# Performance work log

Hardware: AMD Instinct MI355X
Metric: run time of the kernel (lower is better)

## Reference

```python
import jax, jax.numpy as jnp
import numpy as np

N = 100000
E = 1600000
D = 64


def setup_inputs() -> dict:
    key = jax.random.key(0)
    k1, k2 = jax.random.split(key)
    x = jax.random.normal(k1, (N, D), dtype=jnp.float32)
    lambda_ = jnp.ones((), dtype=jnp.float32)  # nn.Parameter init 1.0
    edge_index = jax.random.randint(k2, (2, E), 0, N, dtype=jnp.int64)
    return {"input": x, "lambda_": lambda_, "edge_index": edge_index}


def reference(input, lambda_, edge_index):
    # actual lambda = 1 + relu(lambda_)
    lam = 1.0 + jax.nn.relu(lambda_)
    v1 = (2.0 * lam - 2.0) / lam  # self-loop weight
    v2 = 2.0 / lam                # neighbor edge weight
    row = edge_index[0]
    col = edge_index[1]
    # SpMM: out[r] = v1 * x[r] + v2 * sum_{(r,c) in E} x[c]
    nbr = jax.ops.segment_sum(input[col], row, num_segments=N)  # [N, D]
    agg = v1 * input + v2 * nbr
    # row-sum normalization: rowsum[r] = v1 + v2 * deg(r)
    deg = jax.ops.segment_sum(jnp.ones((E,), dtype=input.dtype), row, num_segments=N)
    rowsum = v1 + v2 * deg  # [N]
    return agg / rowsum[:, None]
```

## Files before the change

### kernel.cpp

```cpp
#include <hip/hip_runtime.h>

#define NN 100000
#define NE 1600000
#define DD 64

#define RSH 9
#define RPB 512
#define NBUCK 196
#define CAP 8704
#define CH2 8192
#define EPB 16
#define NABLK ((NE + CH2 - 1) / CH2)
#define CONV_TOT (NN * DD / 8)

__device__ __forceinline__ void get_v(const float* __restrict__ lam_p, float& v1, float& v2) {
    float l = lam_p[0];
    float lam = 1.0f + (l > 0.0f ? l : 0.0f);
    v1 = (2.0f * lam - 2.0f) / lam;
    v2 = 2.0f / lam;
}

__device__ __forceinline__ float bf2f(unsigned short u) {
    return __uint_as_float(((unsigned)u) << 16);
}

__device__ __forceinline__ void conv8(const float* __restrict__ x, unsigned short* __restrict__ xb, int i) {
    float4 a = reinterpret_cast<const float4*>(x)[2 * i];
    float4 b = reinterpret_cast<const float4*>(x)[2 * i + 1];
    float f[8] = {a.x, a.y, a.z, a.w, b.x, b.y, b.z, b.w};
#pragma unroll
    for (int j = 0; j < 4; ++j) {
        unsigned u0 = __float_as_uint(f[2 * j]);
        unsigned u1 = __float_as_uint(f[2 * j + 1]);
        u0 = (u0 + 0x7FFFu + ((u0 >> 16) & 1u)) >> 16;
        u1 = (u1 + 0x7FFFu + ((u1 >> 16) & 1u)) >> 16;
        unsigned packed = u0 | (u1 << 16);
        __builtin_nontemporal_store(packed, reinterpret_cast<unsigned*>(xb) + 4 * i + j);
    }
}

__global__ __launch_bounds__(512) void bucketA_kernel(const int* __restrict__ ei,
                                                      const float* __restrict__ x,
                                                      unsigned short* __restrict__ xb,
                                                      int* __restrict__ bcursor,
                                                      unsigned int* __restrict__ slab) {
    __shared__ unsigned int stage[CH2];
    __shared__ unsigned char sbuck[CH2];
    __shared__ unsigned int hist[256];
    __shared__ unsigned int lstart[256];
    __shared__ unsigned int lcur[256];
    __shared__ unsigned int gbase[256];
    __shared__ unsigned int scanbuf[512];
    int tid = threadIdx.x;
    long base = (long)blockIdx.x * CH2;

    int rr[EPB];
#pragma unroll
    for (int i = 0; i < EPB; ++i) {
        long e = base + i * 512 + tid;
        rr[i] = (e < NE) ? ei[e] : -1;
    }
    unsigned pv[EPB];
    unsigned char bk[EPB];
    unsigned char ok[EPB];
#pragma unroll
    for (int i = 0; i < EPB; ++i) {
        long e = base + i * 512 + tid;
        int c = (e < NE) ? ei[NE + e] : 0;
        if (rr[i] >= 0) {
            unsigned bb = (unsigned)rr[i] >> RSH;
            bk[i] = (unsigned char)bb;
            ok[i] = 1;
            pv[i] = (((unsigned)rr[i] & (RPB - 1u)) << 17) | (unsigned)c;
        } else { bk[i] = 0; ok[i] = 0; pv[i] = 0u; }
    }

    {
        const int per_blk = (CONV_TOT + NABLK - 1) / NABLK;
        int cs = blockIdx.x * per_blk;
        int ce = cs + per_blk; if (ce > CONV_TOT) ce = CONV_TOT;
        for (int i = cs + tid; i < ce; i += 512) conv8(x, xb, i);
    }

    for (int i = tid; i < 256; i += 512) hist[i] = 0u;
    __syncthreads();
#pragma unroll
    for (int i = 0; i < EPB; ++i)
        if (ok[i]) atomicAdd(&hist[bk[i]], 1u);
    __syncthreads();
    unsigned v = (tid < 256) ? hist[tid] : 0u;
    scanbuf[tid] = v;
    __syncthreads();
    for (int off = 1; off < 512; off <<= 1) {
        unsigned t = (tid >= off) ? scanbuf[tid - off] : 0u;
        __syncthreads();
        scanbuf[tid] += t;
        __syncthreads();
    }
    if (tid < NBUCK) {
        unsigned excl = scanbuf[tid] - v;
        lstart[tid] = excl;
        lcur[tid]   = excl;
        gbase[tid]  = (unsigned)(tid * CAP) + (unsigned)atomicAdd(&bcursor[tid], (int)v);
    }
    __syncthreads();
#pragma unroll
    for (int i = 0; i < EPB; ++i) {
        if (!ok[i]) continue;
        unsigned p = atomicAdd(&lcur[bk[i]], 1u);
        stage[p] = pv[i];
        sbuck[p] = bk[i];
    }
    __syncthreads();
    int tot = (int)((base + CH2 <= NE) ? CH2 : (NE - base));
    for (int k = tid; k < tot; k += 512) {
        unsigned bb = sbuck[k];
        unsigned dst = gbase[bb] + (unsigned)k - lstart[bb];
        if (dst < (bb + 1u) * CAP) slab[dst] = stage[k];
    }
}

__global__ __launch_bounds__(512) void bucketB_kernel(const int* __restrict__ bcursor,
                                                      unsigned int* __restrict__ slab,
                                                      unsigned int* __restrict__ rstartp) {
    __shared__ unsigned int stg[CAP];
    __shared__ unsigned int scanbuf[RPB];
    __shared__ int lcur[RPB];
    __shared__ unsigned int hist[RPB];
    int tid = threadIdx.x;
    int b = blockIdx.x;
    int cnt = bcursor[b];
    if (cnt > CAP) cnt = CAP;
    unsigned int* slab_b = slab + (unsigned)b * CAP;

    for (int k = tid; k < cnt; k += 512) stg[k] = slab_b[k];
    hist[tid] = 0u;
    __syncthreads();
    for (int k = tid; k < cnt; k += 512) atomicAdd(&hist[stg[k] >> 17], 1u);
    __syncthreads();
    unsigned v = hist[tid];
    scanbuf[tid] = v;
    __syncthreads();
    for (int off = 1; off < 512; off <<= 1) {
        unsigned t = (tid >= off) ? scanbuf[tid - off] : 0u;
        __syncthreads();
        scanbuf[tid] += t;
        __syncthreads();
    }
    unsigned excl = scanbuf[tid] - v;
    int row = b * RPB + tid;
    if (row < NN) rstartp[row] = ((unsigned)(b * CAP) + excl) | (v << 21);
    lcur[tid] = (int)excl;
    __syncthreads();
    for (int k = tid; k < cnt; k += 512) {
        unsigned pv = stg[k];
        int rl = (int)(pv >> 17);
        int pos = atomicAdd(&lcur[rl], 1);
        slab_b[pos] = pv & 0x1FFFFu;
    }
}

__global__ void gather_kernel(const unsigned short* __restrict__ xb,
                              const float* __restrict__ lam,
                              const unsigned int* __restrict__ rstartp,
                              const unsigned int* __restrict__ slab,
                              float* __restrict__ out) {
    int wid  = (blockIdx.x * blockDim.x + threadIdx.x) >> 6;
    int lane = threadIdx.x & 63;
    if (wid >= NN) return;
    unsigned rp = rstartp[wid];
    int s  = __builtin_amdgcn_readfirstlane((int)(rp & 0x1FFFFFu));
    int dg = __builtin_amdgcn_readfirstlane((int)(rp >> 21));
    int e  = s + dg;
    float v1, v2; get_v(lam, v1, v2);
    float acc0 = 0.f, acc1 = 0.f, acc2 = 0.f, acc3 = 0.f;
    int k = s;
    for (; k + 16 <= e; k += 16) {
        unsigned myc = slab[k + (lane & 15)];
        float vv[16];
#pragma unroll
        for (int q = 0; q < 16; ++q) {
            int c = __builtin_amdgcn_readlane((int)myc, q);
            vv[q] = bf2f(xb[(size_t)(unsigned)c * DD + lane]);
        }
        acc0 += (vv[0] + vv[4]) + (vv[8]  + vv[12]);
        acc1 += (vv[1] + vv[5]) + (vv[9]  + vv[13]);
        acc2 += (vv[2] + vv[6]) + (vv[10] + vv[14]);
        acc3 += (vv[3] + vv[7]) + (vv[11] + vv[15]);
    }
    if (k + 8 <= e) {
        unsigned myc = slab[k + (lane & 7)];
        float vv[8];
#pragma unroll
        for (int q = 0; q < 8; ++q) {
            int c = __builtin_amdgcn_readlane((int)myc, q);
            vv[q] = bf2f(xb[(size_t)(unsigned)c * DD + lane]);
        }
        acc0 += vv[0] + vv[4];
        acc1 += vv[1] + vv[5];
        acc2 += vv[2] + vv[6];
        acc3 += vv[3] + vv[7];
        k += 8;
    }
    if (k + 4 <= e) {
        unsigned myc = slab[k + (lane & 3)];
        float vv[4];
#pragma unroll
        for (int q = 0; q < 4; ++q) {
            int c = __builtin_amdgcn_readlane((int)myc, q);
            vv[q] = bf2f(xb[(size_t)(unsigned)c * DD + lane]);
        }
        acc0 += vv[0]; acc1 += vv[1]; acc2 += vv[2]; acc3 += vv[3];
        k += 4;
    }
    for (; k < e; ++k) {
        int c = __builtin_amdgcn_readfirstlane((int)slab[k]);
        acc0 += bf2f(xb[(size_t)(unsigned)c * DD + lane]);
    }
    float acc  = (acc0 + acc1) + (acc2 + acc3);
    int swid = __builtin_amdgcn_readfirstlane(wid);
    float self = bf2f(xb[(size_t)swid * DD + lane]);
    float r = (v1 * self + v2 * acc) / (v1 + v2 * (float)dg);
    __builtin_nontemporal_store(r, &out[(size_t)swid * DD + lane]);
}

extern "C" void kernel_launch(void* const* d_in, const int* in_sizes, int n_in,
                              void* d_out, int out_size, void* d_ws, size_t ws_size,
                              hipStream_t stream) {
    const float* x   = (const float*)d_in[0];
    const float* lam = (const float*)d_in[1];
    const int*   ei  = (const int*)d_in[2];
    float* out = (float*)d_out;

    int* ws = (int*)d_ws;
    int* bcursor            = ws;
    unsigned int* rstartp   = (unsigned int*)(ws + 512);
    unsigned int* slab      = rstartp + NN;
    unsigned short* xb      = (unsigned short*)(slab + (size_t)NBUCK * CAP);

    hipMemsetAsync(bcursor, 0, 512 * sizeof(int), stream);

    bucketA_kernel<<<NABLK, 512, 0, stream>>>(ei, x, xb, bcursor, slab);
    bucketB_kernel<<<NBUCK, 512, 0, stream>>>(bcursor, slab, rstartp);

    long tG = (long)NN * 64;
    gather_kernel<<<(int)((tG + 255) / 256), 256, 0, stream>>>(xb, lam, rstartp, slab, out);
}
```

Before: 89.79 us.

## Gather 8 neighbors per wave with 16-byte bf16 row loads and shuffle reduction

Restructures the gather so each wave splits into 8 groups of 8 lanes. Each group loads a whole 128-byte bf16 neighbor row as uint4 vectors, and the partial sums are combined with xor-shuffles across groups. It replaces the old per-lane 2-byte loads with readlane broadcasts, which is meant to cut load instruction count and raise bytes per request. The self term now reads the fp32 input directly, and v2 is folded into the accumulation. In exchange it adds shuffle-reduction work and masked-off iterations for rows whose degree is not a multiple of 8, and only 8 lanes perform the final store.

```diff
diff --git a/kernel.cpp b/kernel.cpp
--- a/kernel.cpp
+++ b/kernel.cpp
@@ -13,15 +13,13 @@
 #define NABLK ((NE + CH2 - 1) / CH2)
 #define CONV_TOT (NN * DD / 8)
 
+typedef float f32x4 __attribute__((ext_vector_type(4)));
+
 __device__ __forceinline__ void get_v(const float* __restrict__ lam_p, float& v1, float& v2) {
     float l = lam_p[0];
     float lam = 1.0f + (l > 0.0f ? l : 0.0f);
     v1 = (2.0f * lam - 2.0f) / lam;
     v2 = 2.0f / lam;
-}
-
-__device__ __forceinline__ float bf2f(unsigned short u) {
-    return __uint_as_float(((unsigned)u) << 16);
 }
 
 __device__ __forceinline__ void conv8(const float* __restrict__ x, unsigned short* __restrict__ xb, int i) {
@@ -161,6 +159,7 @@
 }
 
 __global__ void gather_kernel(const unsigned short* __restrict__ xb,
+                              const float* __restrict__ x,
                               const float* __restrict__ lam,
                               const unsigned int* __restrict__ rstartp,
                               const unsigned int* __restrict__ slab,
@@ -169,59 +168,64 @@
     int lane = threadIdx.x & 63;
     if (wid >= NN) return;
     unsigned rp = rstartp[wid];
-    int s  = __builtin_amdgcn_readfirstlane((int)(rp & 0x1FFFFFu));
-    int dg = __builtin_amdgcn_readfirstlane((int)(rp >> 21));
+    int s  = (int)(rp & 0x1FFFFFu);
+    int dg = (int)(rp >> 21);
     int e  = s + dg;
     float v1, v2; get_v(lam, v1, v2);
-    float acc0 = 0.f, acc1 = 0.f, acc2 = 0.f, acc3 = 0.f;
-    int k = s;
-    for (; k + 16 <= e; k += 16) {
-        unsigned myc = slab[k + (lane & 15)];
-        float vv[16];
-#pragma unroll
-        for (int q = 0; q < 16; ++q) {
-            int c = __builtin_amdgcn_readlane((int)myc, q);
-            vv[q] = bf2f(xb[(size_t)(unsigned)c * DD + lane]);
+    int grp = lane >> 3, sub = lane & 7;
+
+    float a0 = 0.f, a1 = 0.f, a2 = 0.f, a3 = 0.f, a4 = 0.f, a5 = 0.f, a6 = 0.f, a7 = 0.f;
+    for (int k0 = s; k0 < e; k0 += 64) {
+        int idx = k0 + lane; int emax = e - 1;
+        if (idx > emax) idx = emax;
+        unsigned myc = slab[idx];
+        int rem = e - k0; if (rem > 64) rem = 64;
+        for (int k = 0; k < rem; k += 8) {
+            int src = k + grp;
+            unsigned cg = __shfl(myc, src, 64);
+            unsigned c = cg & 0x1FFFFu;
+            if (c >= NN) c = 0;
+            float m = (src < rem) ? v2 : 0.0f;
+            uint4 d = *(reinterpret_cast<const uint4*>(xb + (size_t)c * DD) + sub);
+            a0 = fmaf(__uint_as_float(d.x << 16),          m, a0);
+            a1 = fmaf(__uint_as_float(d.x & 0xFFFF0000u),  m, a1);
+            a2 = fmaf(__uint_as_float(d.y << 16),          m, a2);
+            a3 = fmaf(__uint_as_float(d.y & 0xFFFF0000u),  m, a3);
+            a4 = fmaf(__uint_as_float(d.z << 16),          m, a4);
+            a5 = fmaf(__uint_as_float(d.z & 0xFFFF0000u),  m, a5);
+            a6 = fmaf(__uint_as_float(d.w << 16),          m, a6);
+            a7 = fmaf(__uint_as_float(d.w & 0xFFFF0000u),  m, a7);
         }
-        acc0 += (vv[0] + vv[4]) + (vv[8]  + vv[12]);
-        acc1 += (vv[1] + vv[5]) + (vv[9]  + vv[13]);
-        acc2 += (vv[2] + vv[6]) + (vv[10] + vv[14]);
-        acc3 += (vv[3] + vv[7]) + (vv[11] + vv[15]);
-    }
-    if (k + 8 <= e) {
-        unsigned myc = slab[k + (lane & 7)];
-        float vv[8];
-#pragma unroll
-        for (int q = 0; q < 8; ++q) {
-            int c = __builtin_amdgcn_readlane((int)myc, q);
-            vv[q] = bf2f(xb[(size_t)(unsigned)c * DD + lane]);
-        }
-        acc0 += vv[0] + vv[4];
-        acc1 += vv[1] + vv[5];
-        acc2 += vv[2] + vv[6];
-        acc3 += vv[3] + vv[7];
-        k += 8;
-    }
-    if (k + 4 <= e) {
-        unsigned myc = slab[k + (lane & 3)];
-        float vv[4];
-#pragma unroll
-        for (int q = 0; q < 4; ++q) {
-            int c = __builtin_amdgcn_readlane((int)myc, q);
-            vv[q] = bf2f(xb[(size_t)(unsigned)c * DD + lane]);
-        }
-        acc0 += vv[0]; acc1 += vv[1]; acc2 += vv[2]; acc3 += vv[3];
-        k += 4;
-    }
-    for (; k < e; ++k) {
-        int c = __builtin_amdgcn_readfirstlane((int)slab[k]);
-        acc0 += bf2f(xb[(size_t)(unsigned)c * DD + lane]);
-    }
-    float acc  = (acc0 + acc1) + (acc2 + acc3);
-    int swid = __builtin_amdgcn_readfirstlane(wid);
-    float self = bf2f(xb[(size_t)swid * DD + lane]);
-    float r = (v1 * self + v2 * acc) / (v1 + v2 * (float)dg);
-    __builtin_nontemporal_store(r, &out[(size_t)swid * DD + lane]);
+    }
+#pragma unroll
+    for (int mm = 8; mm <= 32; mm <<= 1) {
+        a0 += __shfl_xor(a0, mm, 64);
+        a1 += __shfl_xor(a1, mm, 64);
+        a2 += __shfl_xor(a2, mm, 64);
+        a3 += __shfl_xor(a3, mm, 64);
+        a4 += __shfl_xor(a4, mm, 64);
+        a5 += __shfl_xor(a5, mm, 64);
+        a6 += __shfl_xor(a6, mm, 64);
+        a7 += __shfl_xor(a7, mm, 64);
+    }
+    const float* xr = x + (size_t)wid * DD + sub * 8;
+    float4 sx0 = *reinterpret_cast<const float4*>(xr);
+    float4 sx1 = *reinterpret_cast<const float4*>(xr + 4);
+    float inv = 1.0f / (v1 + v2 * (float)dg);
+    f32x4 w0, w1;
+    w0.x = (v1 * sx0.x + a0) * inv;
+    w0.y = (v1 * sx0.y + a1) * inv;
+    w0.z = (v1 * sx0.z + a2) * inv;
+    w0.w = (v1 * sx0.w + a3) * inv;
+    w1.x = (v1 * sx1.x + a4) * inv;
+    w1.y = (v1 * sx1.y + a5) * inv;
+    w1.z = (v1 * sx1.z + a6) * inv;
+    w1.w = (v1 * sx1.w + a7) * inv;
+    if (grp == 0) {
+        float* orow = out + (size_t)wid * DD + sub * 8;
+        __builtin_nontemporal_store(w0, reinterpret_cast<f32x4*>(orow));
+        __builtin_nontemporal_store(w1, reinterpret_cast<f32x4*>(orow + 4));
+    }
 }
 
 extern "C" void kernel_launch(void* const* d_in, const int* in_sizes, int n_in,
@@ -244,5 +248,5 @@
     bucketB_kernel<<<NBUCK, 512, 0, stream>>>(bcursor, slab, rstartp);
 
     long tG = (long)NN * 64;
-    gather_kernel<<<(int)((tG + 255) / 256), 256, 0, stream>>>(xb, lam, rstartp, slab, out);
-}
+    gather_kernel<<<(int)((tG + 255) / 256), 256, 0, stream>>>(xb, x, lam, rstartp, slab, out);
+}
```

Measured after the change: 89.14 us. About the same (-0.7%).
